# Kernel tuning notes

Measured on AMD Instinct MI355X. Metric: run time of the kernel, lower is better.

## Reference

```python
import jax, jax.numpy as jnp
import numpy as np

D_MODEL = 512
D_INNER = 1024
SEQ_LEN = 512
BATCH = 16


def _layernorm(x, g, b, eps=1e-5):
    mu = jnp.mean(x, axis=-1, keepdims=True)
    var = jnp.mean(jnp.square(x - mu), axis=-1, keepdims=True)
    return (x - mu) * jax.lax.rsqrt(var + eps) * g + b


def setup_inputs() -> dict:
    key = jax.random.key(0)
    ks = jax.random.split(key, 10)
    dm, D, L = D_MODEL, D_INNER, SEQ_LEN
    s = lambda k, shape, scale: jax.random.normal(k, shape, jnp.float32) * scale
    return {
        "x": jax.random.normal(ks[0], (BATCH, L, dm), jnp.float32),
        "in_proj_w": s(ks[1], (2 * D, dm), dm ** -0.5),
        "in_proj_b": jnp.zeros((2 * D,), jnp.float32),
        "ln1_g": jnp.ones((D,), jnp.float32),
        "ln1_b": jnp.zeros((D,), jnp.float32),
        "conv_w": s(ks[2], (D, D, 3), (3 * D) ** -0.5),  # OIL layout
        "conv_b": jnp.zeros((D,), jnp.float32),
        "A": s(ks[3], (D, D), 0.5 * D ** -0.5),  # spectral radius ~0.5 for stability
        "B": s(ks[4], (D, D), D ** -0.5),
        "C": s(ks[5], (D, D), D ** -0.5),
        "ln2_g": jnp.ones((D,), jnp.float32),
        "ln2_b": jnp.zeros((D,), jnp.float32),
        "out_w": s(ks[6], (D, D), D ** -0.5),
        "out_b": jnp.zeros((D,), jnp.float32),
    }


def reference(x, in_proj_w, in_proj_b, ln1_g, ln1_b, conv_w, conv_b,
              A, B, C, ln2_g, ln2_b, out_w, out_b):
    D = A.shape[0]
    b = x.shape[0]
    proj = x @ in_proj_w.T + in_proj_b               # (b, l, 2D)
    xs, res = proj[..., :D], proj[..., D:]
    xn = _layernorm(xs, ln1_g, ln1_b)
    # conv1d over length with kernel 3, padding 1 (NCL layout)
    xc = jax.lax.conv_general_dilated(
        xn.transpose(0, 2, 1), conv_w, window_strides=(1,), padding=[(1, 1)],
        dimension_numbers=("NCL", "OIL", "NCL")) + conv_b[None, :, None]
    xc = jax.nn.silu(xc).transpose(0, 2, 1)          # (b, l, D)
    # dropout: eval-mode identity

    def step(h, x_t):
        h = h @ A + x_t @ B                          # (b, D)
        return h, h @ C

    h0 = jnp.zeros((b, D), x.dtype)
    _, ys = jax.lax.scan(step, h0, xc.transpose(1, 0, 2))  # ys: (l, b, D)
    y = ys.transpose(1, 0, 2) * jax.nn.silu(res)
    y = _layernorm(y, ln2_g, ln2_b)
    y = y @ out_w.T + out_b + xc
    return y.reshape(b, -1)
```

## Files before the change

kernel.cpp:

```cpp
#include <hip/hip_runtime.h>
#include <stdint.h>

typedef unsigned short u16;
typedef u16   u16x4 __attribute__((ext_vector_type(4)));
typedef float f32x4 __attribute__((ext_vector_type(4)));
typedef short short8 __attribute__((ext_vector_type(8)));

__device__ __forceinline__ float b2f(u16 h){
  union { unsigned int u; float f; } v; v.u = ((unsigned int)h) << 16; return v.f;
}
__device__ __forceinline__ u16 f2b(float f){
  union { float f; unsigned int u; } v; v.f = f;
  unsigned int r = v.u + 0x7FFFu + ((v.u >> 16) & 1u);
  return (u16)(r >> 16);
}
__device__ __forceinline__ float silu_f(float x){ return x / (1.f + __expf(-x)); }

__device__ __forceinline__ void gll16(const u16* g, u16* l){
  __builtin_amdgcn_global_load_lds(
      (__attribute__((address_space(1))) void*)(uintptr_t)(const void*)g,
      (__attribute__((address_space(3))) void*)(void*)l, 16, 0, 0);
}

template<int EPI, int T>
__global__ __launch_bounds__(256) void gemm_k(
    const u16* __restrict__ A, const u16* __restrict__ B,
    int K, int lda, int extra,
    const float* __restrict__ bias, const u16* __restrict__ ebf,
    u16* __restrict__ O1, u16* __restrict__ O2, float* __restrict__ Of, int oextra)
{
  constexpr int FR = T / 32;
  constexpr int NQ = T / 32;
  __shared__ u16 lA[2][T*64];
  __shared__ u16 lB[2][T*64];
  const int tid = threadIdx.x, lane = tid & 63, wv = tid >> 6;
  const int wr = wv >> 1, wc = wv & 1;

  int bx = blockIdx.x, by = blockIdx.y;
  {
    const int gx = gridDim.x;
    const int nwg = gx * gridDim.y;
    if ((nwg & 7) == 0) {
      const int wg = by * gx + bx;
      const int q = nwg >> 3;
      const int swz = (wg & 7) * q + (wg >> 3);
      bx = swz % gx; by = swz / gx;
    }
  }
  const int m0 = by * T, n0 = bx * T;
  const int lr = lane & 15;
  const int g4 = lane >> 4;
  f32x4 acc[FR][FR] = {};

  auto stage = [&](int bsel, int k0) {
    #pragma unroll
    for (int q = 0; q < NQ; q++) {
      int e  = q*2048 + tid*8;
      int r  = e >> 6;
      int s  = (e >> 3) & 7;
      int cs = ((s ^ (r & 7)) << 3);
      int ra = m0 + r;
      long long ia = (long long)ra*lda + (long long)(ra>>9)*extra + (k0 + cs);
      gll16(A + ia, &lA[bsel][q*2048 + wv*512]);
      gll16(B + (long long)(n0 + r)*K + (k0 + cs), &lB[bsel][q*2048 + wv*512]);
    }
  };

  const int nt = K >> 6;
  stage(0, 0);
  for (int t = 0; t < nt; ++t) {
    const int cur = t & 1;
    __syncthreads();
    if (t + 1 < nt) stage(cur ^ 1, (t + 1) << 6);
    const u16* la = lA[cur];
    const u16* lb = lB[cur];
    #pragma unroll
    for (int kk = 0; kk < 2; kk++) {
      short8 af[FR], bg[FR];
      const int ss = g4 + kk*4;
      #pragma unroll
      for (int i = 0; i < FR; i++) {
        int rowA = wr*(T/2) + i*16 + lr;
        af[i] = *(const short8*)&la[rowA*64 + ((ss ^ (rowA & 7)) << 3)];
      }
      #pragma unroll
      for (int i = 0; i < FR; i++) {
        int rowB = wc*(T/2) + i*16 + lr;
        bg[i] = *(const short8*)&lb[rowB*64 + ((ss ^ (rowB & 7)) << 3)];
      }
      #pragma unroll
      for (int mi = 0; mi < FR; mi++)
        #pragma unroll
        for (int ni = 0; ni < FR; ni++)
          acc[mi][ni] = __builtin_amdgcn_mfma_f32_16x16x32_bf16(af[mi], bg[ni], acc[mi][ni], 0, 0, 0);
    }
  }

  const int rb = m0 + wr*(T/2) + (g4 << 2);
  const int cb = n0 + wc*(T/2) + lr;
  #pragma unroll
  for (int mi = 0; mi < FR; mi++) {
    #pragma unroll
    for (int ni = 0; ni < FR; ni++) {
      #pragma unroll
      for (int r = 0; r < 4; r++) {
        int row = rb + mi*16 + r;
        int col = cb + ni*16;
        float v = acc[mi][ni][r];
        size_t ro = (size_t)row*1024 + (size_t)(row >> 9)*oextra + col;
        if constexpr (EPI == 0) {
          v += bias[col];
          if (col < 1024) O1[(size_t)row*1024 + col] = f2b(v);
          else            O2[(size_t)row*1024 + (col - 1024)] = f2b(v);
        } else if constexpr (EPI == 1) {
          O1[ro] = f2b(silu_f(v + bias[col]));
        } else if constexpr (EPI == 2) {
          O1[ro] = f2b(v);
        } else if constexpr (EPI == 3) {
          O1[ro] = f2b(v * silu_f(b2f(ebf[ro])));
        } else if constexpr (EPI == 4) {
          Of[ro] = v + bias[col] + b2f(ebf[ro]);
        } else {
          O1[ro] = f2b(v + b2f(ebf[ro]));
        }
      }
    }
  }
}

__global__ __launch_bounds__(256) void zpad_k(u16* __restrict__ p, int bstride, int rstart)
{
  u16x4* d = (u16x4*)(p + (size_t)blockIdx.y * bstride + (size_t)(rstart + blockIdx.x) * 1024);
  u16x4 z = {0, 0, 0, 0};
  d[threadIdx.x] = z;
}

__global__ __launch_bounds__(256) void ln_k(
    const u16* __restrict__ in, const float* __restrict__ gw, const float* __restrict__ bw,
    u16* __restrict__ out, int pad)
{
  const int m = blockIdx.x;
  const int t4 = threadIdx.x * 4;
  const u16* row = in + (size_t)m * 1024;
  u16x4 v = *(const u16x4*)&row[t4];
  float x0 = b2f(v[0]), x1 = b2f(v[1]), x2 = b2f(v[2]), x3 = b2f(v[3]);
  float s = x0 + x1 + x2 + x3;
  float q = x0*x0 + x1*x1 + x2*x2 + x3*x3;
  #pragma unroll
  for (int off = 32; off > 0; off >>= 1) { s += __shfl_down(s, off); q += __shfl_down(q, off); }
  __shared__ float ps[4], pq[4];
  const int wv = threadIdx.x >> 6, lane = threadIdx.x & 63;
  if (lane == 0) { ps[wv] = s; pq[wv] = q; }
  __syncthreads();
  s = ps[0] + ps[1] + ps[2] + ps[3];
  q = pq[0] + pq[1] + pq[2] + pq[3];
  float mu  = s * 0.0009765625f;
  float var = q * 0.0009765625f - mu * mu;
  float rs  = rsqrtf(var + 1e-5f);
  f32x4 g4 = *(const f32x4*)&gw[t4];
  f32x4 b4 = *(const f32x4*)&bw[t4];
  size_t orow = pad ? (size_t)((m >> 9)*514 + (m & 511) + 1) : (size_t)m;
  u16x4 o;
  o[0] = f2b((x0 - mu)*rs*g4[0] + b4[0]);
  o[1] = f2b((x1 - mu)*rs*g4[1] + b4[1]);
  o[2] = f2b((x2 - mu)*rs*g4[2] + b4[2]);
  o[3] = f2b((x3 - mu)*rs*g4[3] + b4[3]);
  *(u16x4*)&out[orow*1024 + t4] = o;
}

__global__ __launch_bounds__(256) void cast_k(const float* __restrict__ in, u16* __restrict__ out, int n4)
{
  int i = blockIdx.x*256 + threadIdx.x;
  if (i < n4) {
    f32x4 v = *(const f32x4*)&in[(size_t)i*4];
    u16x4 o; o[0]=f2b(v[0]); o[1]=f2b(v[1]); o[2]=f2b(v[2]); o[3]=f2b(v[3]);
    *(u16x4*)&out[(size_t)i*4] = o;
  }
}

__global__ __launch_bounds__(256) void tcast_k(const float* __restrict__ in, u16* __restrict__ out)
{
  __shared__ float tile[32][33];
  const int tx = threadIdx.x & 31, ty = threadIdx.x >> 5;
  const int c0 = blockIdx.x * 32, r0 = blockIdx.y * 32;
  #pragma unroll
  for (int j = 0; j < 4; j++)
    tile[ty + j*8][tx] = in[(size_t)(r0 + ty + j*8)*1024 + c0 + tx];
  __syncthreads();
  #pragma unroll
  for (int j = 0; j < 4; j++)
    out[(size_t)(c0 + ty + j*8)*1024 + r0 + tx] = f2b(tile[tx][ty + j*8]);
}

__global__ __launch_bounds__(256) void btrans_k(const u16* __restrict__ in, u16* __restrict__ out)
{
  __shared__ u16 tile[32][33];
  const int tx = threadIdx.x & 31, ty = threadIdx.x >> 5;
  const int c0 = blockIdx.x * 32, r0 = blockIdx.y * 32;
  #pragma unroll
  for (int j = 0; j < 4; j++)
    tile[ty + j*8][tx] = in[(size_t)(r0 + ty + j*8)*1024 + c0 + tx];
  __syncthreads();
  #pragma unroll
  for (int j = 0; j < 4; j++)
    out[(size_t)(c0 + ty + j*8)*1024 + r0 + tx] = tile[tx][ty + j*8];
}

__global__ __launch_bounds__(256) void wconv_k(const float* __restrict__ in, u16* __restrict__ out)
{
  int idx = blockIdx.x*256 + threadIdx.x;
  int o   = idx / 3072;
  int rem = idx - o*3072;
  int kk  = rem >> 10;
  int i   = rem & 1023;
  out[idx] = f2b(in[(size_t)o*3072 + i*3 + kk]);
}

extern "C" void kernel_launch(void* const* d_in, const int* in_sizes, int n_in,
                              void* d_out, int out_size, void* d_ws, size_t ws_size,
                              hipStream_t stream)
{
  const float* x   = (const float*)d_in[0];
  const float* w1  = (const float*)d_in[1];
  const float* b1  = (const float*)d_in[2];
  const float* g1  = (const float*)d_in[3];
  const float* be1 = (const float*)d_in[4];
  const float* wcv = (const float*)d_in[5];
  const float* cb  = (const float*)d_in[6];
  const float* Am  = (const float*)d_in[7];
  const float* Bm  = (const float*)d_in[8];
  const float* Cm  = (const float*)d_in[9];
  const float* g2  = (const float*)d_in[10];
  const float* be2 = (const float*)d_in[11];
  const float* wo  = (const float*)d_in[12];
  const float* bo  = (const float*)d_in[13];
  float* out = (float*)d_out;
  (void)in_sizes; (void)n_in; (void)out_size; (void)ws_size;

  char* ws = (char*)d_ws;
  u16* xbf  = (u16*)(ws + 0);
  u16* w1b  = (u16*)(ws + 8388608);
  u16* wcb  = (u16*)(ws + 10485760);
  u16* P1   = (u16*)(ws + 0);
  u16* Acast= (u16*)(ws + 17039360);
  u16* T1   = (u16*)(ws + 19136512);
  u16* T2   = (u16*)(ws + 21233664);
  u16* R2   = (u16*)(ws + 23330816);
  u16* T4   = (u16*)(ws + 25427968);
  u16* R4   = (u16*)(ws + 27525120);
  u16* T8   = (u16*)(ws + 29622272);
  u16* Btb  = (u16*)(ws + 31719424);
  u16* Ctb  = (u16*)(ws + 33816576);
  u16* wob  = (u16*)(ws + 35913728);
  u16* xsb  = (u16*)(ws + 38010880);
  u16* resb = (u16*)(ws + 54788096);
  u16* P0   = (u16*)(ws + 71565312);
  u16* xcb = xsb;
  u16* yb  = P1;
  u16* zb  = resb;
  u16* P0r = P0 + 8192;
  u16* P1r = P1 + 8192;
  const int PE = 8192;

  cast_k<<<4096, 256, 0, stream>>>(x,  xbf, 1048576);
  cast_k<<<1024, 256, 0, stream>>>(w1, w1b, 262144);
  cast_k<<<1024, 256, 0, stream>>>(wo, wob, 262144);
  cast_k<<<1024, 256, 0, stream>>>(Am, Acast, 262144);
  wconv_k<<<12288, 256, 0, stream>>>(wcv, wcb);
  dim3 tg(32, 32);
  tcast_k<<<tg, 256, 0, stream>>>(Am, T1);
  tcast_k<<<tg, 256, 0, stream>>>(Bm, Btb);
  tcast_k<<<tg, 256, 0, stream>>>(Cm, Ctb);

  gemm_k<0,128><<<dim3(16,64), 256, 0, stream>>>(xbf, w1b, 512, 512, 0,
                                                 b1, nullptr, xsb, resb, nullptr, 0);

  gemm_k<2,64><<<dim3(16,16), 256, 0, stream>>>(T1, Acast, 1024, 1024, 0,
                                                nullptr, nullptr, T2, nullptr, nullptr, 0);
  btrans_k<<<tg, 256, 0, stream>>>(T2, R2);
  gemm_k<2,64><<<dim3(16,16), 256, 0, stream>>>(T2, R2, 1024, 1024, 0,
                                                nullptr, nullptr, T4, nullptr, nullptr, 0);
  btrans_k<<<tg, 256, 0, stream>>>(T4, R4);
  gemm_k<2,64><<<dim3(16,16), 256, 0, stream>>>(T4, R4, 1024, 1024, 0,
                                                nullptr, nullptr, T8, nullptr, nullptr, 0);

  zpad_k<<<dim3(1,16), 256, 0, stream>>>(P0, 514*1024, 0);
  zpad_k<<<dim3(1,16), 256, 0, stream>>>(P0, 514*1024, 513);
  ln_k<<<8192, 256, 0, stream>>>(xsb, g1, be1, P0, 1);
  gemm_k<1,128><<<dim3(8,64), 256, 0, stream>>>(P0, wcb, 3072, 1024, 2048,
                                                cb, nullptr, xcb, nullptr, nullptr, 0);
  zpad_k<<<dim3(8,16), 256, 0, stream>>>(P0, 520*1024, 0);
  zpad_k<<<dim3(8,16), 256, 0, stream>>>(P1, 520*1024, 0);
  gemm_k<2,128><<<dim3(8,64), 256, 0, stream>>>(xcb, Btb, 1024, 1024, 0,
                                                nullptr, nullptr, P0r, nullptr, nullptr, PE);
  gemm_k<5,128><<<dim3(8,64), 256, 0, stream>>>(P0r - 1024, T1, 1024, 1024, PE,
                                                nullptr, P0r, P1r, nullptr, nullptr, PE);
  gemm_k<5,128><<<dim3(8,64), 256, 0, stream>>>(P1r - 2048, T2, 1024, 1024, PE,
                                                nullptr, P1r, P0r, nullptr, nullptr, PE);
  gemm_k<5,128><<<dim3(8,64), 256, 0, stream>>>(P0r - 4096, T4, 1024, 1024, PE,
                                                nullptr, P0r, P1r, nullptr, nullptr, PE);
  gemm_k<5,128><<<dim3(8,64), 256, 0, stream>>>(P1r - 8192, T8, 1024, 1024, PE,
                                                nullptr, P1r, P0r, nullptr, nullptr, PE);
  gemm_k<3,128><<<dim3(8,64), 256, 0, stream>>>(P0r, Ctb, 1024, 1024, PE,
                                                nullptr, resb, yb, nullptr, nullptr, 0);
  ln_k<<<8192, 256, 0, stream>>>(yb, g2, be2, zb, 0);
  gemm_k<4,128><<<dim3(8,64), 256, 0, stream>>>(zb, wob, 1024, 1024, 0,
                                                bo, xcb, nullptr, nullptr, out, 0);
}
```

Baseline: 345.1 us.

## Replace async global-to-LDS double buffer with register-staged single LDS buffer

The GEMM kernel drops the direct global_load_lds double-buffered staging. It now prefetches the next K tile into registers, writes them to a single swizzled LDS buffer, and adds a second barrier per iteration. This halves LDS use and sets launch_bounds occupancy to 3 blocks, which should allow more resident workgroups. In exchange it adds register pressure, an extra sync each step, and explicit LDS stores.

```diff
diff --git a/kernel.cpp b/kernel.cpp
--- a/kernel.cpp
+++ b/kernel.cpp
@@ -3,6 +3,7 @@
 
 typedef unsigned short u16;
 typedef u16   u16x4 __attribute__((ext_vector_type(4)));
+typedef u16   u16x8 __attribute__((ext_vector_type(8)));
 typedef float f32x4 __attribute__((ext_vector_type(4)));
 typedef short short8 __attribute__((ext_vector_type(8)));
 
@@ -16,14 +17,8 @@
 }
 __device__ __forceinline__ float silu_f(float x){ return x / (1.f + __expf(-x)); }
 
-__device__ __forceinline__ void gll16(const u16* g, u16* l){
-  __builtin_amdgcn_global_load_lds(
-      (__attribute__((address_space(1))) void*)(uintptr_t)(const void*)g,
-      (__attribute__((address_space(3))) void*)(void*)l, 16, 0, 0);
-}
-
 template<int EPI, int T>
-__global__ __launch_bounds__(256) void gemm_k(
+__global__ __launch_bounds__(256, 3) void gemm_k(
     const u16* __restrict__ A, const u16* __restrict__ B,
     int K, int lda, int extra,
     const float* __restrict__ bias, const u16* __restrict__ ebf,
@@ -31,8 +26,8 @@
 {
   constexpr int FR = T / 32;
   constexpr int NQ = T / 32;
-  __shared__ u16 lA[2][T*64];
-  __shared__ u16 lB[2][T*64];
+  __shared__ u16 lA[T*64];
+  __shared__ u16 lB[T*64];
   const int tid = threadIdx.x, lane = tid & 63, wv = tid >> 6;
   const int wr = wv >> 1, wc = wv & 1;
 
@@ -51,29 +46,37 @@
   const int lr = lane & 15;
   const int g4 = lane >> 4;
   f32x4 acc[FR][FR] = {};
-
-  auto stage = [&](int bsel, int k0) {
+  u16x8 av[NQ], bv[NQ];
+
+  auto preload = [&](int k0) {
+    #pragma unroll
+    for (int q = 0; q < NQ; q++) {
+      int e  = q*2048 + tid*8;
+      int r  = e >> 6;
+      int c  = e & 63;
+      long long ra = m0 + r;
+      av[q] = *(const u16x8*)(A + ra*lda + (ra>>9)*(long long)extra + (k0 + c));
+      bv[q] = *(const u16x8*)(B + (long long)(n0 + r)*K + (k0 + c));
+    }
+  };
+  auto commit = [&]() {
     #pragma unroll
     for (int q = 0; q < NQ; q++) {
       int e  = q*2048 + tid*8;
       int r  = e >> 6;
       int s  = (e >> 3) & 7;
-      int cs = ((s ^ (r & 7)) << 3);
-      int ra = m0 + r;
-      long long ia = (long long)ra*lda + (long long)(ra>>9)*extra + (k0 + cs);
-      gll16(A + ia, &lA[bsel][q*2048 + wv*512]);
-      gll16(B + (long long)(n0 + r)*K + (k0 + cs), &lB[bsel][q*2048 + wv*512]);
+      int off = r*64 + ((s ^ (r & 7)) << 3);
+      *(u16x8*)&lA[off] = av[q];
+      *(u16x8*)&lB[off] = bv[q];
     }
   };
 
   const int nt = K >> 6;
-  stage(0, 0);
+  preload(0);
   for (int t = 0; t < nt; ++t) {
-    const int cur = t & 1;
+    commit();
     __syncthreads();
-    if (t + 1 < nt) stage(cur ^ 1, (t + 1) << 6);
-    const u16* la = lA[cur];
-    const u16* lb = lB[cur];
+    if (t + 1 < nt) preload((t + 1) << 6);
     #pragma unroll
     for (int kk = 0; kk < 2; kk++) {
       short8 af[FR], bg[FR];
@@ -81,12 +84,12 @@
       #pragma unroll
       for (int i = 0; i < FR; i++) {
         int rowA = wr*(T/2) + i*16 + lr;
-        af[i] = *(const short8*)&la[rowA*64 + ((ss ^ (rowA & 7)) << 3)];
+        af[i] = *(const short8*)&lA[rowA*64 + ((ss ^ (rowA & 7)) << 3)];
       }
       #pragma unroll
       for (int i = 0; i < FR; i++) {
         int rowB = wc*(T/2) + i*16 + lr;
-        bg[i] = *(const short8*)&lb[rowB*64 + ((ss ^ (rowB & 7)) << 3)];
+        bg[i] = *(const short8*)&lB[rowB*64 + ((ss ^ (rowB & 7)) << 3)];
       }
       #pragma unroll
       for (int mi = 0; mi < FR; mi++)
@@ -94,6 +97,7 @@
         for (int ni = 0; ni < FR; ni++)
           acc[mi][ni] = __builtin_amdgcn_mfma_f32_16x16x32_bf16(af[mi], bg[ni], acc[mi][ni], 0, 0, 0);
     }
+    __syncthreads();
   }
 
   const int rb = m0 + wr*(T/2) + (g4 << 2);
```

New measurement: 351.1 us. No clear change (+1.7%).
